# Optimization experiments

Measured on AMD Instinct MI355X. Metric: run time of the kernel, lower is better.

The kernel has to match this reference:

```python
import jax, jax.numpy as jnp
import numpy as np

RES = 32
EPS = 0.0


def setup_inputs() -> dict:
    key = jax.random.key(0)
    k1, k2 = jax.random.split(key)
    B, C, N = 32, 64, 8192
    features = jax.random.normal(k1, (B, C, N), dtype=jnp.float32)
    coords = jax.random.normal(k2, (B, 3, N), dtype=jnp.float32)
    return {"features": features, "coords": coords}


def reference(features, coords):
    R = RES
    B, C, N = features.shape
    # center coords per batch (mean over points)
    norm_coords = coords - jnp.mean(coords, axis=2, keepdims=True)  # [B,3,N]
    # normalize=True branch: divide by 2*max point L2 norm
    max_norm = jnp.max(jnp.linalg.norm(norm_coords, axis=1, keepdims=True),
                       axis=2, keepdims=True)  # [B,1,1]
    norm_coords = norm_coords / (max_norm * 2.0 + EPS) + 0.5
    # scale to voxel grid and clip
    norm_coords = jnp.clip(norm_coords * R, 0.0, R - 1)  # [B,3,N]
    vox = jnp.round(norm_coords).astype(jnp.int32)  # [B,3,N]
    # flat voxel index per point, offset per batch -> global segment id
    flat = (vox[:, 0] * R + vox[:, 1]) * R + vox[:, 2]  # [B,N]
    idx = (flat + jnp.arange(B, dtype=jnp.int32)[:, None] * (R ** 3)).reshape(-1)  # [B*N]
    num_seg = B * R ** 3
    cnt = jax.ops.segment_sum(jnp.ones((B * N,), features.dtype), idx,
                              num_segments=num_seg)  # [B*R^3]
    feat_pn = features.transpose(0, 2, 1).reshape(B * N, C)  # [B*N,C]
    sums = jax.ops.segment_sum(feat_pn, idx, num_segments=num_seg)  # [B*R^3,C]
    avg = sums / jnp.maximum(cnt, 1.0)[:, None]
    voxelized = avg.reshape(B, R, R, R, C).transpose(0, 4, 1, 2, 3)  # [B,C,R,R,R]
    return voxelized, norm_coords
```

## Files before the change

### kernel.cpp

```cpp
#include <hip/hip_runtime.h>

constexpr int B = 32, C = 64, N = 8192, R = 32, R3 = R * R * R;
constexpr int HALF = R3 / 2;
constexpr int T = 1024;
constexpr int PPT = N / T;

constexpr size_t CNT_OFF = 0;
constexpr size_t IDX_OFF = (size_t)B * R3 * 4;
constexpr size_t PF_OFF  = IDX_OFF + (size_t)B * N * 2;
constexpr size_t PRM_OFF = PF_OFF + (size_t)B * N * 4;

__device__ __forceinline__ void lds_barrier() {
  asm volatile("s_waitcnt lgkmcnt(0)" ::: "memory");
  __builtin_amdgcn_s_barrier();
  __builtin_amdgcn_sched_barrier(0);
}

__global__ __launch_bounds__(1024) void stats_kernel(
    const float* __restrict__ coords, float* __restrict__ params,
    unsigned int* __restrict__ cnt) {
  const int b = blockIdx.x;
  const int t = threadIdx.x;
  const float* cb = coords + (size_t)b * 3 * N;
  __shared__ double sm[1024];
  __shared__ float smf[1024];

  {
    uint4* cz = (uint4*)(cnt + (size_t)b * R3);
    const uint4 z4 = {0u, 0u, 0u, 0u};
#pragma unroll
    for (int k = 0; k < R3 / 4; k += 1024) cz[k + t] = z4;
  }

  double sx = 0.0, sy = 0.0, sz = 0.0;
  for (int n = t; n < N; n += 1024) {
    sx += (double)cb[n];
    sy += (double)cb[N + n];
    sz += (double)cb[2 * N + n];
  }
  float mean[3];
  double vals[3] = {sx, sy, sz};
  for (int d = 0; d < 3; ++d) {
    sm[t] = vals[d];
    __syncthreads();
    for (int s = 512; s > 0; s >>= 1) {
      if (t < s) sm[t] += sm[t + s];
      __syncthreads();
    }
    mean[d] = (float)(sm[0] / (double)N);
    __syncthreads();
  }

  float mx = 0.0f;
  for (int n = t; n < N; n += 1024) {
    float dx = __fsub_rn(cb[n], mean[0]);
    float dy = __fsub_rn(cb[N + n], mean[1]);
    float dz = __fsub_rn(cb[2 * N + n], mean[2]);
    float n2 = __fadd_rn(__fadd_rn(__fmul_rn(dx, dx), __fmul_rn(dy, dy)),
                         __fmul_rn(dz, dz));
    mx = fmaxf(mx, n2);
  }
  smf[t] = mx;
  __syncthreads();
  for (int s = 512; s > 0; s >>= 1) {
    if (t < s) smf[t] = fmaxf(smf[t], smf[t + s]);
    __syncthreads();
  }
  if (t == 0) {
    float maxn = __fsqrt_rn(smf[0]);
    params[b * 4 + 0] = mean[0];
    params[b * 4 + 1] = mean[1];
    params[b * 4 + 2] = mean[2];
    params[b * 4 + 3] = __fmul_rn(maxn, 2.0f);
  }
}

__global__ __launch_bounds__(256) void voxelize_kernel(
    const float* __restrict__ coords, const float* __restrict__ params,
    float* __restrict__ ncout, unsigned short* __restrict__ idx,
    unsigned int* __restrict__ cnt) {
  const int i = blockIdx.x * 256 + threadIdx.x;
  const int b = i >> 13;
  const int n = i & (N - 1);
  const float* cb = coords + (size_t)b * 3 * N;
  const float m0 = params[b * 4 + 0];
  const float m1 = params[b * 4 + 1];
  const float m2 = params[b * 4 + 2];
  const float dn = params[b * 4 + 3];

  float t0 = __fmul_rn(__fadd_rn(__fdiv_rn(__fsub_rn(cb[n], m0), dn), 0.5f), 32.0f);
  float t1 = __fmul_rn(__fadd_rn(__fdiv_rn(__fsub_rn(cb[N + n], m1), dn), 0.5f), 32.0f);
  float t2 = __fmul_rn(__fadd_rn(__fdiv_rn(__fsub_rn(cb[2 * N + n], m2), dn), 0.5f), 32.0f);
  t0 = fminf(fmaxf(t0, 0.0f), 31.0f);
  t1 = fminf(fmaxf(t1, 0.0f), 31.0f);
  t2 = fminf(fmaxf(t2, 0.0f), 31.0f);

  ncout[(size_t)b * 3 * N + n] = t0;
  ncout[(size_t)b * 3 * N + N + n] = t1;
  ncout[(size_t)b * 3 * N + 2 * N + n] = t2;

  const int vx = (int)rintf(t0);
  const int vy = (int)rintf(t1);
  const int vz = (int)rintf(t2);
  const int flat = (vx * R + vy) * R + vz;
  idx[i] = (unsigned short)flat;
  atomicAdd(&cnt[b * R3 + flat], 1u);
}

__global__ __launch_bounds__(256) void invp_kernel(
    const unsigned short* __restrict__ idx,
    const unsigned int* __restrict__ cnt, float* __restrict__ pf) {
  const int i = blockIdx.x * 256 + threadIdx.x;
  const int b = i >> 13;
  const unsigned int k = cnt[b * R3 + (int)idx[i]];
  pf[i] = __fdiv_rn(1.0f, (float)(k ? k : 1u));
}

__global__ __launch_bounds__(1024, 8) void accum_kernel(
    const float* __restrict__ feats, const unsigned short* __restrict__ idx,
    const float* __restrict__ pf, float* __restrict__ voxout) {
  __shared__ float lds[HALF];
  const int blk = blockIdx.x;
  const int c = blk & (C - 1);
  const int b = blk >> 6;
  const int t = threadIdx.x;

  const unsigned short* ib = idx + (size_t)b * N;
  const float* pb = pf + (size_t)b * N;
  const float* fb = feats + ((size_t)b * C + c) * N;
  int iv[PPT];
  float fv[PPT];
#pragma unroll
  for (int k = 0; k < PPT; ++k) {
    const int n = t + k * T;
    iv[k] = (int)ib[n];
    fv[k] = fb[n] * pb[n];
  }

  float4* lp = (float4*)lds;
  const float4 z = {0.f, 0.f, 0.f, 0.f};

  for (int h = 0; h < 2; ++h) {
    const int lo = h * HALF;

#pragma unroll
    for (int k = t; k < HALF / 4; k += T) lp[k] = z;
    lds_barrier();

#pragma unroll
    for (int k = 0; k < PPT; ++k) {
      const int loc = iv[k] - lo;
      if ((unsigned)loc < (unsigned)HALF) atomicAdd(&lds[loc], fv[k]);
    }
    lds_barrier();

    float4* ob4 = (float4*)(voxout + ((size_t)b * C + c) * R3 + lo);
#pragma unroll
    for (int v = t; v < HALF / 4; v += T) ob4[v] = lp[v];
    if (h == 0) lds_barrier();
  }
}

extern "C" void kernel_launch(void* const* d_in, const int* in_sizes, int n_in,
                              void* d_out, int out_size, void* d_ws,
                              size_t ws_size, hipStream_t stream) {
  const float* feats  = (const float*)d_in[0];
  const float* coords = (const float*)d_in[1];

  float* voxout = (float*)d_out;
  float* ncout  = voxout + (size_t)B * C * R3;

  char* ws = (char*)d_ws;
  unsigned int* cnt   = (unsigned int*)(ws + CNT_OFF);
  unsigned short* idx = (unsigned short*)(ws + IDX_OFF);
  float* pf           = (float*)(ws + PF_OFF);
  float* params       = (float*)(ws + PRM_OFF);

  stats_kernel<<<B, 1024, 0, stream>>>(coords, params, cnt);
  voxelize_kernel<<<(B * N) / 256, 256, 0, stream>>>(coords, params, ncout,
                                                     idx, cnt);
  invp_kernel<<<(B * N) / 256, 256, 0, stream>>>(idx, cnt, pf);
  accum_kernel<<<B * C, 1024, 0, stream>>>(feats, idx, pf, voxout);
}
```

Measured before the change: 378.0 us.

## Fuse stats, voxelize and inverse-count kernels into one per-batch prep kernel

Merges the three preprocessing kernels into a single kernel with one block per batch. Per-voxel counts move from a global array with global atomics into a 128KB LDS histogram with shared-memory atomics, so the global count buffer and its zeroing go away. It also removes two kernel launches and the params round trip. The cost is that the prep phase now runs on only 32 blocks, so the voxelize work has less parallelism, and the large LDS allocation limits occupancy.

New measurement: 368.8 us. -2.4%, faster.

```diff
diff --git a/kernel.cpp b/kernel.cpp
--- a/kernel.cpp
+++ b/kernel.cpp
@@ -5,10 +5,8 @@
 constexpr int T = 1024;
 constexpr int PPT = N / T;
 
-constexpr size_t CNT_OFF = 0;
-constexpr size_t IDX_OFF = (size_t)B * R3 * 4;
-constexpr size_t PF_OFF  = IDX_OFF + (size_t)B * N * 2;
-constexpr size_t PRM_OFF = PF_OFF + (size_t)B * N * 4;
+constexpr size_t IDX_OFF = 0;
+constexpr size_t PF_OFF  = (size_t)B * N * 2;
 
 __device__ __forceinline__ void lds_barrier() {
   asm volatile("s_waitcnt lgkmcnt(0)" ::: "memory");
@@ -16,24 +14,20 @@
   __builtin_amdgcn_sched_barrier(0);
 }
 
-__global__ __launch_bounds__(1024) void stats_kernel(
-    const float* __restrict__ coords, float* __restrict__ params,
-    unsigned int* __restrict__ cnt) {
+__global__ __launch_bounds__(1024) void prep_kernel(
+    const float* __restrict__ coords, float* __restrict__ ncout,
+    unsigned short* __restrict__ idx, float* __restrict__ pf) {
+  __shared__ __align__(16) unsigned char smem[R3 * 4];
+  double* sm = (double*)smem;
+  float* smf = (float*)smem;
+  unsigned int* cnt = (unsigned int*)smem;
+
   const int b = blockIdx.x;
   const int t = threadIdx.x;
   const float* cb = coords + (size_t)b * 3 * N;
-  __shared__ double sm[1024];
-  __shared__ float smf[1024];
-
-  {
-    uint4* cz = (uint4*)(cnt + (size_t)b * R3);
-    const uint4 z4 = {0u, 0u, 0u, 0u};
-#pragma unroll
-    for (int k = 0; k < R3 / 4; k += 1024) cz[k + t] = z4;
-  }
 
   double sx = 0.0, sy = 0.0, sz = 0.0;
-  for (int n = t; n < N; n += 1024) {
+  for (int n = t; n < N; n += T) {
     sx += (double)cb[n];
     sy += (double)cb[N + n];
     sz += (double)cb[2 * N + n];
@@ -52,7 +46,7 @@
   }
 
   float mx = 0.0f;
-  for (int n = t; n < N; n += 1024) {
+  for (int n = t; n < N; n += T) {
     float dx = __fsub_rn(cb[n], mean[0]);
     float dy = __fsub_rn(cb[N + n], mean[1]);
     float dz = __fsub_rn(cb[2 * N + n], mean[2]);
@@ -66,54 +60,47 @@
     if (t < s) smf[t] = fmaxf(smf[t], smf[t + s]);
     __syncthreads();
   }
-  if (t == 0) {
-    float maxn = __fsqrt_rn(smf[0]);
-    params[b * 4 + 0] = mean[0];
-    params[b * 4 + 1] = mean[1];
-    params[b * 4 + 2] = mean[2];
-    params[b * 4 + 3] = __fmul_rn(maxn, 2.0f);
+  const float dn = __fmul_rn(__fsqrt_rn(smf[0]), 2.0f);
+  __syncthreads();
+
+  {
+    uint4* cz = (uint4*)cnt;
+    const uint4 z4 = {0u, 0u, 0u, 0u};
+#pragma unroll
+    for (int k = 0; k < R3 / 4; k += T) cz[k + t] = z4;
   }
-}
+  lds_barrier();
 
-__global__ __launch_bounds__(256) void voxelize_kernel(
-    const float* __restrict__ coords, const float* __restrict__ params,
-    float* __restrict__ ncout, unsigned short* __restrict__ idx,
-    unsigned int* __restrict__ cnt) {
-  const int i = blockIdx.x * 256 + threadIdx.x;
-  const int b = i >> 13;
-  const int n = i & (N - 1);
-  const float* cb = coords + (size_t)b * 3 * N;
-  const float m0 = params[b * 4 + 0];
-  const float m1 = params[b * 4 + 1];
-  const float m2 = params[b * 4 + 2];
-  const float dn = params[b * 4 + 3];
+  int iv[PPT];
+#pragma unroll
+  for (int k = 0; k < PPT; ++k) {
+    const int n = t + k * T;
+    float t0 = __fmul_rn(__fadd_rn(__fdiv_rn(__fsub_rn(cb[n], mean[0]), dn), 0.5f), 32.0f);
+    float t1 = __fmul_rn(__fadd_rn(__fdiv_rn(__fsub_rn(cb[N + n], mean[1]), dn), 0.5f), 32.0f);
+    float t2 = __fmul_rn(__fadd_rn(__fdiv_rn(__fsub_rn(cb[2 * N + n], mean[2]), dn), 0.5f), 32.0f);
+    t0 = fminf(fmaxf(t0, 0.0f), 31.0f);
+    t1 = fminf(fmaxf(t1, 0.0f), 31.0f);
+    t2 = fminf(fmaxf(t2, 0.0f), 31.0f);
 
-  float t0 = __fmul_rn(__fadd_rn(__fdiv_rn(__fsub_rn(cb[n], m0), dn), 0.5f), 32.0f);
-  float t1 = __fmul_rn(__fadd_rn(__fdiv_rn(__fsub_rn(cb[N + n], m1), dn), 0.5f), 32.0f);
-  float t2 = __fmul_rn(__fadd_rn(__fdiv_rn(__fsub_rn(cb[2 * N + n], m2), dn), 0.5f), 32.0f);
-  t0 = fminf(fmaxf(t0, 0.0f), 31.0f);
-  t1 = fminf(fmaxf(t1, 0.0f), 31.0f);
-  t2 = fminf(fmaxf(t2, 0.0f), 31.0f);
+    ncout[(size_t)b * 3 * N + n] = t0;
+    ncout[(size_t)b * 3 * N + N + n] = t1;
+    ncout[(size_t)b * 3 * N + 2 * N + n] = t2;
 
-  ncout[(size_t)b * 3 * N + n] = t0;
-  ncout[(size_t)b * 3 * N + N + n] = t1;
-  ncout[(size_t)b * 3 * N + 2 * N + n] = t2;
+    const int vx = (int)rintf(t0);
+    const int vy = (int)rintf(t1);
+    const int vz = (int)rintf(t2);
+    const int flat = (vx * R + vy) * R + vz;
+    iv[k] = flat;
+    idx[(size_t)b * N + n] = (unsigned short)flat;
+    atomicAdd(&cnt[flat], 1u);
+  }
+  lds_barrier();
 
-  const int vx = (int)rintf(t0);
-  const int vy = (int)rintf(t1);
-  const int vz = (int)rintf(t2);
-  const int flat = (vx * R + vy) * R + vz;
-  idx[i] = (unsigned short)flat;
-  atomicAdd(&cnt[b * R3 + flat], 1u);
-}
-
-__global__ __launch_bounds__(256) void invp_kernel(
-    const unsigned short* __restrict__ idx,
-    const unsigned int* __restrict__ cnt, float* __restrict__ pf) {
-  const int i = blockIdx.x * 256 + threadIdx.x;
-  const int b = i >> 13;
-  const unsigned int k = cnt[b * R3 + (int)idx[i]];
-  pf[i] = __fdiv_rn(1.0f, (float)(k ? k : 1u));
+#pragma unroll
+  for (int k = 0; k < PPT; ++k) {
+    const int n = t + k * T;
+    pf[(size_t)b * N + n] = __fdiv_rn(1.0f, (float)cnt[iv[k]]);
+  }
 }
 
 __global__ __launch_bounds__(1024, 8) void accum_kernel(
@@ -171,14 +158,9 @@
   float* ncout  = voxout + (size_t)B * C * R3;
 
   char* ws = (char*)d_ws;
-  unsigned int* cnt   = (unsigned int*)(ws + CNT_OFF);
   unsigned short* idx = (unsigned short*)(ws + IDX_OFF);
   float* pf           = (float*)(ws + PF_OFF);
-  float* params       = (float*)(ws + PRM_OFF);
 
-  stats_kernel<<<B, 1024, 0, stream>>>(coords, params, cnt);
-  voxelize_kernel<<<(B * N) / 256, 256, 0, stream>>>(coords, params, ncout,
-                                                     idx, cnt);
-  invp_kernel<<<(B * N) / 256, 256, 0, stream>>>(idx, cnt, pf);
+  prep_kernel<<<B, 1024, 0, stream>>>(coords, ncout, idx, pf);
   accum_kernel<<<B * C, 1024, 0, stream>>>(feats, idx, pf, voxout);
 }
```
